# Performance work log

Hardware: AMD Instinct MI355X
Metric: run time of the kernel (lower is better)

## Reference

```python
import jax, jax.numpy as jnp
import numpy as np

TH = 0.1        # cfg.th diversity threshold
SL1_BETA = 0.1  # SmoothL1Dis threshold (repo default)
EPS = 1e-8


def setup_inputs() -> dict:
    key = jax.random.key(0)
    ks = jax.random.split(key, 11)
    b, n1, n2, k = 8, 2048, 2048, 128
    f = jnp.float32
    return {
        'pts': jax.random.normal(ks[0], (b, n1, 3), f),
        'recon_delta': jax.random.normal(ks[1], (b, n2, 3), f),
        'pred_kpt_3d': jax.random.normal(ks[2], (b, k, 3), f),
        'recon_model': jax.random.normal(ks[3], (b, n2, 3), f),
        'pred_kpt_nocs': jax.random.normal(ks[4], (b, k, 3), f),
        'pred_rotation': jax.random.normal(ks[5], (b, 3, 3), f),
        'pred_translation': jax.random.normal(ks[6], (b, 3), f),
        'pred_size': jax.random.normal(ks[7], (b, 3), f),
        'rotation_label': jax.random.normal(ks[8], (b, 3, 3), f),
        'translation_label': jax.random.normal(ks[9], (b, 3), f),
        'size_label': jax.random.normal(ks[10], (b, 3), f),
    }


def _pairwise_dist(a, b):
    # a: (B,N,3), b: (B,M,3) -> (B,N,M) euclidean distances
    return jnp.linalg.norm(a[:, :, None, :] - b[:, None, :, :], axis=-1)


def _loss_all(pts, recon_delta, pred_kpt_3d, recon_model, pred_kpt_nocs,
              pred_rotation, pred_translation, pred_size,
              rotation_label, translation_label, size_label):
    b = pts.shape[0]
    # --- PoseDis (non-symmetric path): column-norm of R diff + t/s L2 ---
    loss_pose = (jnp.mean(jnp.linalg.norm(pred_rotation - rotation_label, axis=1))
                 + jnp.mean(jnp.linalg.norm(pred_translation - translation_label, axis=1))
                 + jnp.mean(jnp.linalg.norm(pred_size - size_label, axis=1)))

    # --- bidirectional chamfer pts <-> keypoints (chamfer_dis_k2p) ---
    d_pk = _pairwise_dist(pts, pred_kpt_3d)            # (B, N1, K)
    loss_cd = 0.5 * (jnp.mean(jnp.min(d_pk, axis=1)) + jnp.mean(jnp.min(d_pk, axis=2)))

    # --- NOCS smooth-L1 on GT-transformed keypoints ---
    scale = jnp.linalg.norm(size_label, axis=1).reshape(b, 1, 1) + EPS
    kpt_nocs_gt = jnp.einsum('bki,bij->bkj',
                             (pred_kpt_3d - translation_label[:, None, :]) / scale,
                             rotation_label)
    diff = jnp.abs(pred_kpt_nocs - kpt_nocs_gt)
    sl1 = jnp.where(diff > SL1_BETA, diff - SL1_BETA / 2.0, diff * diff / (2.0 * SL1_BETA))
    loss_nocs = jnp.mean(jnp.sum(sl1, axis=2))

    # --- diversity_loss_3d1: clamp pairwise kpt distances at TH, diag -> inf->TH ---
    kk = pred_kpt_3d.shape[1]
    eye = jnp.eye(kk, dtype=bool)[None]                 # (1, K, K)
    d2 = jnp.sum((pred_kpt_3d[:, :, None, :] - pred_kpt_3d[:, None, :, :]) ** 2, axis=-1)
    d2 = jnp.where(eye, 1.0, d2)                        # safe sqrt on diagonal
    dm = jnp.where(eye, jnp.inf, jnp.sqrt(d2))
    loss_diversity = jnp.mean(jnp.minimum(dm, TH))

    # --- bidirectional chamfer pts <-> recon_model ---
    d_pr = _pairwise_dist(pts, recon_model)             # (B, N1, N2)
    loss_recon = 0.5 * (jnp.mean(jnp.min(d_pr, axis=2)) + jnp.mean(jnp.min(d_pr, axis=1)))

    # --- delta magnitude regularizer ---
    loss_delta = jnp.mean(jnp.linalg.norm(recon_delta, axis=2))

    # cfg weights all 1.0
    return loss_pose + loss_nocs + loss_cd + loss_diversity + loss_recon + loss_delta


def reference(pts, recon_delta, pred_kpt_3d, recon_model, pred_kpt_nocs,
              pred_rotation, pred_translation, pred_size,
              rotation_label, translation_label, size_label):
    return _loss_all(pts, recon_delta, pred_kpt_3d, recon_model, pred_kpt_nocs,
                     pred_rotation, pred_translation, pred_size,
                     rotation_label, translation_label, size_label)
```

## Files before the change

### kernel.cpp

```cpp
#include <hip/hip_runtime.h>
#include <hip/hip_bf16.h>
#include <math.h>

#define BB   8
#define N1   2048
#define N2   2048
#define KK   128
#define TH_  0.1f
#define SL1B 0.1f
#define EPS_ 1e-8f

#define NBLOCKS 413


__global__ __launch_bounds__(256) void loss_mega_kernel(
        const float* __restrict__ pts,
        const float* __restrict__ rdelta,
        const float* __restrict__ kpt,
        const float* __restrict__ recon,
        const float* __restrict__ pnocs,
        const float* __restrict__ prot,
        const float* __restrict__ ptr_,
        const float* __restrict__ psz,
        const float* __restrict__ rl,
        const float* __restrict__ tl,
        const float* __restrict__ sl,
        float* __restrict__ out) {
    __shared__ float4 tile[2048];
    __shared__ float  part[1024];
    __shared__ float  sbuf[4];

    const int blk = blockIdx.x;
    const int t   = threadIdx.x;
    float v = 0.f;

    if (blk < 264) {
        const float *Ap, *Bp;
        int NA, NB, rowbase, b;
        float w;
        if (blk < 128) {
            b = blk >> 4; Ap = pts;  NA = N1; Bp = recon; NB = N2;
            rowbase = (blk & 15) << 7; w = 0.5f / 16384.f;
        } else if (blk < 256) {
            int l = blk - 128;
            b = l >> 4; Ap = recon; NA = N2; Bp = pts; NB = N1;
            rowbase = (l & 15) << 7; w = 0.5f / 16384.f;
        } else {
            b = blk - 256; Ap = kpt; NA = KK; Bp = pts; NB = N1;
            rowbase = 0; w = 0.5f / 1024.f;
        }
        const int scan = NB >> 3;

        for (int j = t; j < NB; j += 256) {
            const float* p = Bp + ((size_t)b * NB + j) * 3;
            float x = p[0], y = p[1], z = p[2];
            tile[j] = make_float4(-2.f * x, -2.f * y, -2.f * z,
                                  x * x + y * y + z * z);
        }
        __syncthreads();

        const int rid = t & 31;
        const int q   = t >> 5;
        float ax[4], ay[4], az[4], asq[4], m[4];
        #pragma unroll
        for (int k = 0; k < 4; ++k) {
            const float* pa = Ap + ((size_t)b * NA + rowbase + rid * 4 + k) * 3;
            ax[k] = pa[0]; ay[k] = pa[1]; az[k] = pa[2];
            asq[k] = ax[k] * ax[k] + ay[k] * ay[k] + az[k] * az[k];
            m[k] = 3.4e38f;
        }

        const int off = q * scan;
        #pragma unroll 4
        for (int j = 0; j < scan; ++j) {
            float4 qv = tile[off + j];
            #pragma unroll
            for (int k = 0; k < 4; ++k) {
                float e = fmaf(ax[k], qv.x,
                          fmaf(ay[k], qv.y,
                          fmaf(az[k], qv.z, qv.w)));
                m[k] = fminf(m[k], e);
            }
        }
        #pragma unroll
        for (int k = 0; k < 4; ++k)
            part[q * 128 + rid * 4 + k] = asq[k] + m[k];
        __syncthreads();
        if (t < 128) {
            float mm = part[t];
            #pragma unroll
            for (int qq = 1; qq < 8; ++qq)
                mm = fminf(mm, part[qq * 128 + t]);
            v = sqrtf(fmaxf(mm, 0.f)) * w;
        }
    } else if (blk < 280) {
        const int l = blk - 264;
        const int b = l >> 1;
        const int rowbase = (l & 1) << 10;
        const float w = 0.5f / 16384.f;

        for (int j = t; j < KK; j += 256) {
            const float* p = kpt + ((size_t)b * KK + j) * 3;
            float x = p[0], y = p[1], z = p[2];
            tile[j] = make_float4(-2.f * x, -2.f * y, -2.f * z,
                                  x * x + y * y + z * z);
        }
        __syncthreads();

        float ax[4], ay[4], az[4], asq[4], m[4];
        #pragma unroll
        for (int k = 0; k < 4; ++k) {
            const float* pa = pts + ((size_t)b * N1 + rowbase + t * 4 + k) * 3;
            ax[k] = pa[0]; ay[k] = pa[1]; az[k] = pa[2];
            asq[k] = ax[k] * ax[k] + ay[k] * ay[k] + az[k] * az[k];
            m[k] = 3.4e38f;
        }
        #pragma unroll 4
        for (int j = 0; j < KK; ++j) {
            float4 qv = tile[j];
            #pragma unroll
            for (int k = 0; k < 4; ++k) {
                float e = fmaf(ax[k], qv.x,
                          fmaf(ay[k], qv.y,
                          fmaf(az[k], qv.z, qv.w)));
                m[k] = fminf(m[k], e);
            }
        }
        float s = 0.f;
        #pragma unroll
        for (int k = 0; k < 4; ++k)
            s += sqrtf(fmaxf(asq[k] + m[k], 0.f));
        v = s * w;
    } else if (blk < 344) {
        const int local = blk - 280;
        float acc = 0.f;
        #pragma unroll
        for (int u = 0; u < 8; ++u) {
            const int g = local * 2048 + u * 256 + t;
            const int b = g >> 14, i = (g >> 7) & 127, j = g & 127;
            const float* pi = kpt + ((size_t)((b << 7) + i)) * 3;
            const float* pj = kpt + ((size_t)((b << 7) + j)) * 3;
            float dx = pi[0] - pj[0], dy = pi[1] - pj[1], dz = pi[2] - pj[2];
            float d2 = dx * dx + dy * dy + dz * dz;
            acc += (i == j) ? TH_ : fminf(sqrtf(d2), TH_);
        }
        v = acc * (1.0f / 131072.0f);
    } else if (blk < 408) {
        const int g = (blk - 344) * 256 + t;
        const float* p = rdelta + (size_t)g * 3;
        v = sqrtf(p[0] * p[0] + p[1] * p[1] + p[2] * p[2]) * (1.0f / 16384.0f);
    } else if (blk < 412) {
        const int g = (blk - 408) * 256 + t;
        const int b = g >> 7, k = g & 127;
        const float* s3 = sl + b * 3;
        float scale = sqrtf(s3[0] * s3[0] + s3[1] * s3[1] + s3[2] * s3[2]) + EPS_;
        const float* t3 = tl + b * 3;
        const float* p3 = kpt + ((size_t)((b << 7) + k)) * 3;
        float p0 = (p3[0] - t3[0]) / scale;
        float p1 = (p3[1] - t3[1]) / scale;
        float p2 = (p3[2] - t3[2]) / scale;
        const float* R = rl + b * 9;
        const float* pn = pnocs + ((size_t)((b << 7) + k)) * 3;
        float s = 0.f;
        #pragma unroll
        for (int j = 0; j < 3; ++j) {
            float gt = p0 * R[j] + p1 * R[3 + j] + p2 * R[6 + j];
            float diff = fabsf(pn[j] - gt);
            s += (diff > SL1B) ? (diff - 0.5f * SL1B) : (diff * diff * (0.5f / SL1B));
        }
        v = s * (1.0f / 1024.0f);
    } else {
        if (t < BB) {
            const int b = t;
            float s = 0.f;
            #pragma unroll
            for (int j = 0; j < 3; ++j) {
                float c = 0.f;
                #pragma unroll
                for (int i = 0; i < 3; ++i) {
                    float d = prot[b * 9 + i * 3 + j] - rl[b * 9 + i * 3 + j];
                    c += d * d;
                }
                s += sqrtf(c);
            }
            v = s * (1.0f / 24.0f);
            float dt2 = 0.f, ds2 = 0.f;
            #pragma unroll
            for (int i = 0; i < 3; ++i) {
                float dt = ptr_[b * 3 + i] - tl[b * 3 + i]; dt2 += dt * dt;
                float ds = psz[b * 3 + i] - sl[b * 3 + i]; ds2 += ds * ds;
            }
            v += (sqrtf(dt2) + sqrtf(ds2)) * (1.0f / 8.0f);
        }
    }

    #pragma unroll
    for (int off = 32; off > 0; off >>= 1)
        v += __shfl_down(v, off, 64);
    if ((t & 63) == 0) sbuf[t >> 6] = v;
    __syncthreads();
    if (t == 0) atomicAdd(out, sbuf[0] + sbuf[1] + sbuf[2] + sbuf[3]);
}

extern "C" void kernel_launch(void* const* d_in, const int* in_sizes, int n_in,
                              void* d_out, int out_size, void* d_ws, size_t ws_size,
                              hipStream_t stream) {
    const float* pts    = (const float*)d_in[0];
    const float* rdelta = (const float*)d_in[1];
    const float* kpt    = (const float*)d_in[2];
    const float* recon  = (const float*)d_in[3];
    const float* pnocs  = (const float*)d_in[4];
    const float* prot   = (const float*)d_in[5];
    const float* ptr_   = (const float*)d_in[6];
    const float* psz    = (const float*)d_in[7];
    const float* rl     = (const float*)d_in[8];
    const float* tl     = (const float*)d_in[9];
    const float* sl     = (const float*)d_in[10];
    float* out = (float*)d_out;

    hipMemsetAsync(d_out, 0, sizeof(float), stream);

    loss_mega_kernel<<<NBLOCKS, 256, 0, stream>>>(
        pts, rdelta, kpt, recon, pnocs, prot, ptr_, psz, rl, tl, sl, out);
}
```

Baseline: 90.83 us.

## Halve rows per block, split scan 16 ways, pad shared tile

Each chamfer block now handles 64 query rows instead of 128, and the 2048-point target tile is scanned in 16 segments of 128 instead of 8 segments of 256. This doubles the block count to 677 so the 256 CUs get more than one wave of work. It also pads the shared tile by one float4 per 128 entries to spread LDS bank access across thread groups. In exchange, each target tile is loaded into shared memory twice as many times overall, and the cross-segment min reduction has more steps.

Result: faster. 87.63 us (-3.5%).

```diff
diff --git a/kernel.cpp b/kernel.cpp
--- a/kernel.cpp
+++ b/kernel.cpp
@@ -10,8 +10,13 @@
 #define SL1B 0.1f
 #define EPS_ 1e-8f
 
-#define NBLOCKS 413
-
+#define NBLOCKS 677
+
+
+#define SCAN  128
+#define TS    129
+#define SPLIT 16
+#define ROWS  64
 
 __global__ __launch_bounds__(256) void loss_mega_kernel(
         const float* __restrict__ pts,
@@ -26,53 +31,54 @@
         const float* __restrict__ tl,
         const float* __restrict__ sl,
         float* __restrict__ out) {
-    __shared__ float4 tile[2048];
-    __shared__ float  part[1024];
+    __shared__ float4 tile[SPLIT * TS];
+    __shared__ float  part[SPLIT * ROWS];
     __shared__ float  sbuf[4];
 
     const int blk = blockIdx.x;
     const int t   = threadIdx.x;
     float v = 0.f;
 
-    if (blk < 264) {
+    if (blk < 528) {
         const float *Ap, *Bp;
-        int NA, NB, rowbase, b;
+        int NA, rowbase, b;
         float w;
-        if (blk < 128) {
-            b = blk >> 4; Ap = pts;  NA = N1; Bp = recon; NB = N2;
-            rowbase = (blk & 15) << 7; w = 0.5f / 16384.f;
-        } else if (blk < 256) {
-            int l = blk - 128;
-            b = l >> 4; Ap = recon; NA = N2; Bp = pts; NB = N1;
-            rowbase = (l & 15) << 7; w = 0.5f / 16384.f;
+        if (blk < 256) {
+            b = blk >> 5; Ap = pts;  NA = N1; Bp = recon;
+            rowbase = (blk & 31) << 6; w = 0.5f / 16384.f;
+        } else if (blk < 512) {
+            int l = blk - 256;
+            b = l >> 5; Ap = recon; NA = N2; Bp = pts;
+            rowbase = (l & 31) << 6; w = 0.5f / 16384.f;
         } else {
-            b = blk - 256; Ap = kpt; NA = KK; Bp = pts; NB = N1;
-            rowbase = 0; w = 0.5f / 1024.f;
-        }
-        const int scan = NB >> 3;
+            int l = blk - 512;
+            b = l >> 1; Ap = kpt; NA = KK; Bp = pts;
+            rowbase = (l & 1) << 6; w = 0.5f / 1024.f;
+        }
+        const int NB = 2048;
 
         for (int j = t; j < NB; j += 256) {
             const float* p = Bp + ((size_t)b * NB + j) * 3;
             float x = p[0], y = p[1], z = p[2];
-            tile[j] = make_float4(-2.f * x, -2.f * y, -2.f * z,
-                                  x * x + y * y + z * z);
+            tile[j + (j >> 7)] = make_float4(-2.f * x, -2.f * y, -2.f * z,
+                                             x * x + y * y + z * z);
         }
         __syncthreads();
 
-        const int rid = t & 31;
-        const int q   = t >> 5;
+        const int g = t & 15;
+        const int q = t >> 4;
         float ax[4], ay[4], az[4], asq[4], m[4];
         #pragma unroll
         for (int k = 0; k < 4; ++k) {
-            const float* pa = Ap + ((size_t)b * NA + rowbase + rid * 4 + k) * 3;
+            const float* pa = Ap + ((size_t)b * NA + rowbase + g * 4 + k) * 3;
             ax[k] = pa[0]; ay[k] = pa[1]; az[k] = pa[2];
             asq[k] = ax[k] * ax[k] + ay[k] * ay[k] + az[k] * az[k];
             m[k] = 3.4e38f;
         }
 
-        const int off = q * scan;
+        const int off = q * TS;
         #pragma unroll 4
-        for (int j = 0; j < scan; ++j) {
+        for (int j = 0; j < SCAN; ++j) {
             float4 qv = tile[off + j];
             #pragma unroll
             for (int k = 0; k < 4; ++k) {
@@ -84,17 +90,17 @@
         }
         #pragma unroll
         for (int k = 0; k < 4; ++k)
-            part[q * 128 + rid * 4 + k] = asq[k] + m[k];
+            part[q * ROWS + g * 4 + k] = asq[k] + m[k];
         __syncthreads();
-        if (t < 128) {
+        if (t < ROWS) {
             float mm = part[t];
             #pragma unroll
-            for (int qq = 1; qq < 8; ++qq)
-                mm = fminf(mm, part[qq * 128 + t]);
+            for (int qq = 1; qq < SPLIT; ++qq)
+                mm = fminf(mm, part[qq * ROWS + t]);
             v = sqrtf(fmaxf(mm, 0.f)) * w;
         }
-    } else if (blk < 280) {
-        const int l = blk - 264;
+    } else if (blk < 544) {
+        const int l = blk - 528;
         const int b = l >> 1;
         const int rowbase = (l & 1) << 10;
         const float w = 0.5f / 16384.f;
@@ -131,13 +137,13 @@
         for (int k = 0; k < 4; ++k)
             s += sqrtf(fmaxf(asq[k] + m[k], 0.f));
         v = s * w;
-    } else if (blk < 344) {
-        const int local = blk - 280;
+    } else if (blk < 608) {
+        const int local = blk - 544;
         float acc = 0.f;
         #pragma unroll
         for (int u = 0; u < 8; ++u) {
-            const int g = local * 2048 + u * 256 + t;
-            const int b = g >> 14, i = (g >> 7) & 127, j = g & 127;
+            const int gg = local * 2048 + u * 256 + t;
+            const int b = gg >> 14, i = (gg >> 7) & 127, j = gg & 127;
             const float* pi = kpt + ((size_t)((b << 7) + i)) * 3;
             const float* pj = kpt + ((size_t)((b << 7) + j)) * 3;
             float dx = pi[0] - pj[0], dy = pi[1] - pj[1], dz = pi[2] - pj[2];
@@ -145,13 +151,13 @@
             acc += (i == j) ? TH_ : fminf(sqrtf(d2), TH_);
         }
         v = acc * (1.0f / 131072.0f);
-    } else if (blk < 408) {
-        const int g = (blk - 344) * 256 + t;
-        const float* p = rdelta + (size_t)g * 3;
+    } else if (blk < 672) {
+        const int gg = (blk - 608) * 256 + t;
+        const float* p = rdelta + (size_t)gg * 3;
         v = sqrtf(p[0] * p[0] + p[1] * p[1] + p[2] * p[2]) * (1.0f / 16384.0f);
-    } else if (blk < 412) {
-        const int g = (blk - 408) * 256 + t;
-        const int b = g >> 7, k = g & 127;
+    } else if (blk < 676) {
+        const int gg = (blk - 672) * 256 + t;
+        const int b = gg >> 7, k = gg & 127;
         const float* s3 = sl + b * 3;
         float scale = sqrtf(s3[0] * s3[0] + s3[1] * s3[1] + s3[2] * s3[2]) + EPS_;
         const float* t3 = tl + b * 3;
```
